# Optimization experiments

Hardware: AMD Instinct MI355X
Metric: run time of the kernel (lower is better)

## Reference

```python
import jax, jax.numpy as jnp
import numpy as np

B, D_IN, LAT, C = 16384, 512, 64, 8
HID = [1024, 512, 256]

def _lin(k, fi, fo, scale=0.02):
    k1, k2 = jax.random.split(k)
    return jax.random.normal(k1, (fi, fo), jnp.float32) * scale, jax.random.normal(k2, (fo,), jnp.float32) * scale

def _lin_c(k, fi, fo, scale=0.02):
    k1, k2 = jax.random.split(k)
    return jax.random.normal(k1, (C, fi, fo), jnp.float32) * scale, jax.random.normal(k2, (C, fo), jnp.float32) * scale

def setup_inputs() -> dict:
    key = jax.random.key(0)
    ks = jax.random.split(key, 16)
    x = jax.random.normal(ks[0], (B, D_IN), jnp.float32)
    cluster_labels = jax.random.randint(ks[1], (B,), 0, C, jnp.int32)
    eps = jax.random.normal(ks[2], (B, LAT), jnp.float32)
    # encoder: shared(512->1024), unshared(1024->512), shared(512->256)
    enc_W0, enc_b0 = _lin(ks[3], D_IN, HID[0])
    enc_Wu, enc_bu = _lin_c(ks[4], HID[0], HID[1])
    enc_W2, enc_b2 = _lin(ks[5], HID[1], HID[2])
    # shared latent heads
    mu_W, mu_b = _lin(ks[6], HID[2], LAT)
    lv_W, lv_b = _lin(ks[7], HID[2], LAT)
    # decoder (hidden_dims reversed = [256,512,1024]): unshared(64->256), shared(256->512), unshared(512->1024)
    dec_Wu0, dec_bu0 = _lin_c(ks[8], LAT, HID[2])
    dec_W1, dec_b1 = _lin(ks[9], HID[2], HID[1])
    dec_Wu2, dec_bu2 = _lin_c(ks[10], HID[1], HID[0])
    # per-cluster final layer (1024 -> input_dim), no activation (all-continuous)
    fin_W, fin_b = _lin_c(ks[11], HID[0], D_IN)
    return dict(x=x, cluster_labels=cluster_labels, eps=eps,
                enc_W0=enc_W0, enc_b0=enc_b0, enc_Wu=enc_Wu, enc_bu=enc_bu,
                enc_W2=enc_W2, enc_b2=enc_b2, mu_W=mu_W, mu_b=mu_b,
                lv_W=lv_W, lv_b=lv_b, dec_Wu0=dec_Wu0, dec_bu0=dec_bu0,
                dec_W1=dec_W1, dec_b1=dec_b1, dec_Wu2=dec_Wu2, dec_bu2=dec_bu2,
                fin_W=fin_W, fin_b=fin_b)

def _unshared(h, W, b, labels):
    # per-cluster GEMM then row-wise combine (mask-based dispatch, no row reorder)
    y = jnp.einsum('bi,cio->bco', h, W) + b[None]  # [B, C, out]
    return jnp.take_along_axis(y, labels[:, None, None], axis=1)[:, 0, :]

def reference(x, cluster_labels, eps,
              enc_W0, enc_b0, enc_Wu, enc_bu, enc_W2, enc_b2,
              mu_W, mu_b, lv_W, lv_b,
              dec_Wu0, dec_bu0, dec_W1, dec_b1, dec_Wu2, dec_bu2,
              fin_W, fin_b):
    lbl = cluster_labels.astype(jnp.int32)
    # encoder
    h = jax.nn.relu(x @ enc_W0 + enc_b0)
    h = jax.nn.relu(_unshared(h, enc_Wu, enc_bu, lbl))
    h = jax.nn.relu(h @ enc_W2 + enc_b2)
    mu = h @ mu_W + mu_b
    logvar = h @ lv_W + lv_b
    # reparameterize
    z = mu + jnp.exp(0.5 * logvar) * eps
    # decoder
    h = jax.nn.relu(_unshared(z, dec_Wu0, dec_bu0, lbl))
    h = jax.nn.relu(h @ dec_W1 + dec_b1)
    h = jax.nn.relu(_unshared(h, dec_Wu2, dec_bu2, lbl))
    # per-cluster final output layer (identity activation: all-continuous)
    recon = _unshared(h, fin_W, fin_b, lbl)
    return recon
```

## Files before the change

kernel.cpp:

```cpp
#include <hip/hip_runtime.h>

typedef _Float16 f16;
typedef __attribute__((ext_vector_type(8))) _Float16 f16x8;
typedef __attribute__((ext_vector_type(4))) _Float16 f16x4;
typedef __attribute__((ext_vector_type(4))) float    f32x4;

#define B_ROWS 16384
#define MPAD   18432
#define MT256  72
#define MT128  144
#define NBLK   64

typedef __attribute__((address_space(1))) void as1_void;
typedef __attribute__((address_space(3))) void as3_void;

__device__ __forceinline__ void gl_lds16(const void* g, void* l) {
    __builtin_amdgcn_global_load_lds((const as1_void*)g, (as3_void*)l, 16, 0, 0);
}


__global__ __launch_bounds__(256) void k_prep(const int* __restrict__ lbl, int* __restrict__ blockhist,
                                              int* __restrict__ rowmap,
                                              const float* __restrict__ mb_, const float* __restrict__ lb_,
                                              float* __restrict__ bz, f16* __restrict__ zerob) {
    int b = blockIdx.x, t = threadIdx.x;
    int i = b * 256 + t;
    rowmap[i] = -1;
    if (b < NBLK) {
        __shared__ int h[8];
        if (t < 8) h[t] = 0;
        __syncthreads();
        atomicAdd(&h[lbl[i]], 1);
        __syncthreads();
        if (t < 8) blockhist[b * 8 + t] = h[t];
    } else if (b == NBLK) {
        if (t < 64) zerob[t] = (f16)0.f;
        if (t < 64) bz[t] = mb_[t];
        else if (t < 128) bz[t] = lb_[t - 64];
    }
}

__global__ void k_offsets(const int* __restrict__ blockhist, int* offs, int* tilec256, int* tilec128,
                          int* blockbase) {
    __shared__ int tot[8];
    __shared__ int so[9];
    int t = threadIdx.x;
    if (t < 8) {
        int s = 0;
        for (int b = 0; b < NBLK; ++b) s += blockhist[b * 8 + t];
        tot[t] = s;
    }
    __syncthreads();
    if (t == 0) {
        int o = 0;
        for (int c = 0; c < 8; ++c) { so[c] = o; o += (tot[c] + 255) & ~255; }
        so[8] = o;
        for (int c = 0; c < 9; ++c) offs[c] = so[c];
    }
    __syncthreads();
    if (t < 8) {
        int run = so[t];
        for (int b = 0; b < NBLK; ++b) {
            blockbase[b * 8 + t] = run;
            run += blockhist[b * 8 + t];
        }
    }
    if (t < MT256) {
        int row = t * 256, c = 7;
        for (int cc = 0; cc < 8; ++cc)
            if (row >= so[cc] && row < so[cc + 1]) c = cc;
        tilec256[t] = c;
    }
    if (t < MT128) {
        int row = t * 128, c = 7;
        for (int cc = 0; cc < 8; ++cc)
            if (row >= so[cc] && row < so[cc + 1]) c = cc;
        tilec128[t] = c;
    }
}

__global__ __launch_bounds__(256) void k_scatter(const int* __restrict__ lbl,
                                                 const int* __restrict__ blockbase,
                                                 int* __restrict__ rowmap) {
    __shared__ int cur[8];
    if (threadIdx.x < 8) cur[threadIdx.x] = blockbase[blockIdx.x * 8 + threadIdx.x];
    __syncthreads();
    int i = blockIdx.x * 256 + threadIdx.x;
    int c = lbl[i];
    int pos = atomicAdd(&cur[c], 1);
    rowmap[pos] = i;
}


struct Seg { const float* s; f16* d; int K, N, b0, nx, ny; long sCS, dCS; };
struct SegTab { Seg g[10]; };

__global__ __launch_bounds__(256) void k_trans(SegTab tab, const float* __restrict__ x, f16* __restrict__ xh) {
    int bid = blockIdx.x;
    int t = threadIdx.x;
    if (bid < tab.g[1].b0) {
        long i = (long)bid * 256 + t;
        const float4* xs = (const float4*)x;
        float4 v0 = xs[i * 2], v1 = xs[i * 2 + 1];
        f16x8 o = {(f16)v0.x, (f16)v0.y, (f16)v0.z, (f16)v0.w,
                   (f16)v1.x, (f16)v1.y, (f16)v1.z, (f16)v1.w};
        ((f16x8*)xh)[i] = o;
        return;
    }
    int s = 9;
    while (bid < tab.g[s].b0) --s;
    Seg sg = tab.g[s];
    int lb = bid - sg.b0;
    int nxy = sg.nx * sg.ny;
    int z = lb / nxy; int r = lb - z * nxy;
    int by = r / sg.nx; int bx = r - by * sg.nx;
    const float* src = sg.s + (size_t)z * sg.sCS;
    f16* dst = sg.d + (size_t)z * sg.dCS;
    int k0 = by * 64, n0 = bx * 64;

    __shared__ f16 tr[64][88];
    int a = t & 15, b = t >> 4;
    float4 v[4];
    #pragma unroll
    for (int i = 0; i < 4; ++i)
        v[i] = *(const float4*)&src[(size_t)(k0 + b * 4 + i) * sg.N + n0 + a * 4];
    #pragma unroll
    for (int j = 0; j < 4; ++j) {
        f16x4 w = {(f16)((const float*)&v[0])[j], (f16)((const float*)&v[1])[j],
                   (f16)((const float*)&v[2])[j], (f16)((const float*)&v[3])[j]};
        *(f16x4*)&tr[a * 4 + j][b * 4] = w;
    }
    __syncthreads();
    int n = t >> 2, s4 = t & 3;
    f16x8 o0 = *(const f16x8*)&tr[n][s4 * 16];
    f16x8 o1 = *(const f16x8*)&tr[n][s4 * 16 + 8];
    *(f16x8*)&dst[(size_t)(n0 + n) * sg.K + k0 + s4 * 16] = o0;
    *(f16x8*)&dst[(size_t)(n0 + n) * sg.K + k0 + s4 * 16 + 8] = o1;
}

__global__ __launch_bounds__(256) void k_reparam(const f16* __restrict__ muv, const float* __restrict__ eps,
                                                 const int* __restrict__ rowmap, f16* __restrict__ z) {
    int i = blockIdx.x * 256 + threadIdx.x;
    int p = i >> 6, j = i & 63;
    int g = rowmap[p];
    float e  = (g >= 0) ? eps[(size_t)g * 64 + j] : 0.f;
    float mu = (float)muv[(size_t)p * 128 + j];
    float lv = (float)muv[(size_t)p * 128 + 64 + j];
    z[i] = (f16)(mu + expf(0.5f * lv) * e);
}


template<int GATHER, int PERW, int RELU, int SCATTER>
__global__ __launch_bounds__(512, 2) void gemm2(
    const f16* __restrict__ A, const f16* __restrict__ Wt,
    const float* __restrict__ bias, f16* __restrict__ Out, float* __restrict__ OutF,
    const int* __restrict__ rowmap, const int* __restrict__ tilec,
    const f16* __restrict__ zerobuf, int K, int N)
{
    __shared__ __align__(16) f16 lA[2][256 * 32];
    __shared__ __align__(16) f16 lB[2][256 * 32];
    const int tid  = threadIdx.x;
    const int wave = tid >> 6;
    const int lane = tid & 63;

    const int id  = blockIdx.x;
    const int xcd = id & 7;
    const int jj  = id >> 3;
    const int tm  = (jj % 9) * 8 + xcd;
    const int tn  = jj / 9;
    const int r0 = tm * 256, n0 = tn * 256;

    const f16* wb = Wt;
    const float* bb = bias;
    if (PERW) {
        int c = tilec[tm];
        wb += (size_t)c * K * N;
        bb += (size_t)c * N;
    }

    const int srow = tid >> 2;
    const int sg   = tid & 3;
    const int xk16 = (sg ^ (srow & 3)) * 16;

    const char* pa[2]; size_t stepA[2];
    #pragma unroll
    for (int p = 0; p < 2; ++p) {
        int gr = r0 + p * 128 + srow;
        if (GATHER) {
            int g = rowmap[gr];
            if (g >= 0) { pa[p] = (const char*)(A + (size_t)g * K) + xk16; stepA[p] = 64; }
            else        { pa[p] = (const char*)zerobuf;                    stepA[p] = 0;  }
        } else {
            pa[p] = (const char*)(A + (size_t)gr * K) + xk16; stepA[p] = 64;
        }
    }
    const char* pb[2];
    #pragma unroll
    for (int p = 0; p < 2; ++p)
        pb[p] = (const char*)(wb + (size_t)(n0 + p * 128 + srow) * K) + xk16;

    const int wm = wave & 3, wn = wave >> 2;
    const int mb = wm * 64, nb = wn * 128;
    const int quad = lane >> 4;
    const int r16  = lane & 15;
    const int key  = r16 & 3;

    f32x4 acc[4][8];
    #pragma unroll
    for (int i = 0; i < 4; ++i)
        #pragma unroll
        for (int j = 0; j < 8; ++j)
            acc[i][j] = (f32x4){0.f, 0.f, 0.f, 0.f};

    const int nk = K >> 5;

    #pragma unroll
    for (int p = 0; p < 2; ++p) {
        gl_lds16(pa[p], (char*)lA[0] + p * 8192 + wave * 1024);
        gl_lds16(pb[p], (char*)lB[0] + p * 8192 + wave * 1024);
        pa[p] += stepA[p]; pb[p] += 64;
    }

    for (int kb = 0; kb < nk; ++kb) {
        const int cur = kb & 1, nxt = cur ^ 1;
        __syncthreads();
        if (kb + 1 < nk) {
            #pragma unroll
            for (int p = 0; p < 2; ++p) {
                gl_lds16(pa[p], (char*)lA[nxt] + p * 8192 + wave * 1024);
                gl_lds16(pb[p], (char*)lB[nxt] + p * 8192 + wave * 1024);
                pa[p] += stepA[p]; pb[p] += 64;
            }
        }
        f16x8 af[4], bf[8];
        #pragma unroll
        for (int i = 0; i < 4; ++i)
            af[i] = *(const f16x8*)((const char*)lA[cur] + (mb + i * 16 + r16) * 64 + ((quad ^ key) * 16));
        #pragma unroll
        for (int j = 0; j < 8; ++j)
            bf[j] = *(const f16x8*)((const char*)lB[cur] + (nb + j * 16 + r16) * 64 + ((quad ^ key) * 16));
        #pragma unroll
        for (int i = 0; i < 4; ++i)
            #pragma unroll
            for (int j = 0; j < 8; ++j)
                acc[i][j] = __builtin_amdgcn_mfma_f32_16x16x32_f16(af[i], bf[j], acc[i][j], 0, 0, 0);
    }

    float bv[8];
    #pragma unroll
    for (int j = 0; j < 8; ++j) bv[j] = bb[n0 + nb + j * 16 + r16];

    #pragma unroll
    for (int i = 0; i < 4; ++i) {
        #pragma unroll
        for (int r = 0; r < 4; ++r) {
            int orow = r0 + mb + i * 16 + quad * 4 + r;
            int g = 0;
            if (SCATTER) g = rowmap[orow];
            #pragma unroll
            for (int j = 0; j < 8; ++j) {
                int ocol = n0 + nb + j * 16 + r16;
                float v = acc[i][j][r] + bv[j];
                if (RELU) v = fmaxf(v, 0.f);
                if (SCATTER) {
                    if (g >= 0) OutF[(size_t)g * N + ocol] = v;
                } else {
                    Out[(size_t)orow * N + ocol] = (f16)v;
                }
            }
        }
    }
}


template<int GATHER, int PERW, int RELU, int SCATTER>
__global__ __launch_bounds__(256, 2) void gemm_k(
    const f16* __restrict__ A, const f16* __restrict__ Wt,
    const float* __restrict__ bias, f16* __restrict__ Out, float* __restrict__ OutF,
    const int* __restrict__ rowmap, const int* __restrict__ tilec,
    const f16* __restrict__ zerobuf, int K, int N)
{
    __shared__ __align__(16) f16 lA[2][128 * 64];
    __shared__ __align__(16) f16 lB[2][128 * 64];
    const int tid  = threadIdx.x;
    const int wave = tid >> 6;
    const int lane = tid & 63;

    const int id  = blockIdx.x;
    const int xcd = id & 7;
    const int jj  = id >> 3;
    const int tm  = (jj % 18) * 8 + xcd;
    const int tn  = jj / 18;
    const int r0 = tm * 128, n0 = tn * 128;

    const f16* wb = Wt;
    const float* bb = bias;
    if (PERW) {
        int c = tilec[tm];
        wb += (size_t)c * K * N;
        bb += (size_t)c * N;
    }

    const int srow = tid >> 3;
    const int sg   = tid & 7;
    const int xk16 = (sg ^ (srow & 7)) * 16;
    const size_t rowB = (size_t)K * 2;
    const size_t passB = 32 * rowB;

    const char* pa[4]; size_t stepA[4];
    #pragma unroll
    for (int p = 0; p < 4; ++p) {
        int gr = r0 + p * 32 + srow;
        if (GATHER) {
            int g = rowmap[gr];
            if (g >= 0) { pa[p] = (const char*)(A + (size_t)g * K) + xk16; stepA[p] = 128; }
            else        { pa[p] = (const char*)zerobuf;                    stepA[p] = 0;   }
        } else {
            pa[p] = (const char*)(A + (size_t)gr * K) + xk16; stepA[p] = 128;
        }
    }
    const char* pb = (const char*)(wb + (size_t)(n0 + srow) * K) + xk16;

    const int mb = (wave >> 1) * 64;
    const int nb = (wave & 1) * 64;
    const int quad = lane >> 4;
    const int r16  = lane & 15;
    const int key  = r16 & 7;

    f32x4 acc[4][4];
    #pragma unroll
    for (int i = 0; i < 4; ++i)
        #pragma unroll
        for (int j = 0; j < 4; ++j)
            acc[i][j] = (f32x4){0.f, 0.f, 0.f, 0.f};

    const int nk = K >> 6;

    #pragma unroll
    for (int p = 0; p < 4; ++p)
        gl_lds16(pa[p], (char*)lA[0] + p * 4096 + wave * 1024);
    #pragma unroll
    for (int p = 0; p < 4; ++p)
        gl_lds16(pb + p * passB, (char*)lB[0] + p * 4096 + wave * 1024);
    #pragma unroll
    for (int p = 0; p < 4; ++p) pa[p] += stepA[p];
    pb += 128;

    for (int kb = 0; kb < nk; ++kb) {
        const int cur = kb & 1, nxt = cur ^ 1;
        __syncthreads();
        if (kb + 1 < nk) {
            #pragma unroll
            for (int p = 0; p < 4; ++p)
                gl_lds16(pa[p], (char*)lA[nxt] + p * 4096 + wave * 1024);
            #pragma unroll
            for (int p = 0; p < 4; ++p)
                gl_lds16(pb + p * passB, (char*)lB[nxt] + p * 4096 + wave * 1024);
            #pragma unroll
            for (int p = 0; p < 4; ++p) pa[p] += stepA[p];
            pb += 128;
        }
        #pragma unroll
        for (int kk = 0; kk < 2; ++kk) {
            const int off = ((kk * 4 + quad) ^ key) * 16;
            f16x8 af[4], bf[4];
            #pragma unroll
            for (int i = 0; i < 4; ++i)
                af[i] = *(const f16x8*)((const char*)lA[cur] + (mb + i * 16 + r16) * 128 + off);
            #pragma unroll
            for (int j = 0; j < 4; ++j)
                bf[j] = *(const f16x8*)((const char*)lB[cur] + (nb + j * 16 + r16) * 128 + off);
            #pragma unroll
            for (int i = 0; i < 4; ++i)
                #pragma unroll
                for (int j = 0; j < 4; ++j)
                    acc[i][j] = __builtin_amdgcn_mfma_f32_16x16x32_f16(af[i], bf[j], acc[i][j], 0, 0, 0);
        }
    }

    float bv[4];
    #pragma unroll
    for (int j = 0; j < 4; ++j) bv[j] = bb[n0 + nb + j * 16 + r16];

    #pragma unroll
    for (int i = 0; i < 4; ++i) {
        #pragma unroll
        for (int r = 0; r < 4; ++r) {
            int orow = r0 + mb + i * 16 + quad * 4 + r;
            int g = 0;
            if (SCATTER) g = rowmap[orow];
            #pragma unroll
            for (int j = 0; j < 4; ++j) {
                int ocol = n0 + nb + j * 16 + r16;
                float v = acc[i][j][r] + bv[j];
                if (RELU) v = fmaxf(v, 0.f);
                if (SCATTER) {
                    if (g >= 0) OutF[(size_t)g * N + ocol] = v;
                } else {
                    Out[(size_t)orow * N + ocol] = (f16)v;
                }
            }
        }
    }
}


extern "C" void kernel_launch(void* const* d_in, const int* in_sizes, int n_in,
                              void* d_out, int out_size, void* d_ws, size_t ws_size,
                              hipStream_t stream) {
    const float* x      = (const float*)d_in[0];
    const int*   lbl    = (const int*)  d_in[1];
    const float* eps    = (const float*)d_in[2];
    const float* enc_W0 = (const float*)d_in[3];
    const float* enc_b0 = (const float*)d_in[4];
    const float* enc_Wu = (const float*)d_in[5];
    const float* enc_bu = (const float*)d_in[6];
    const float* enc_W2 = (const float*)d_in[7];
    const float* enc_b2 = (const float*)d_in[8];
    const float* mu_W   = (const float*)d_in[9];
    const float* mu_b   = (const float*)d_in[10];
    const float* lv_W   = (const float*)d_in[11];
    const float* lv_b   = (const float*)d_in[12];
    const float* dWu0   = (const float*)d_in[13];
    const float* dbu0   = (const float*)d_in[14];
    const float* dW1    = (const float*)d_in[15];
    const float* db1    = (const float*)d_in[16];
    const float* dWu2   = (const float*)d_in[17];
    const float* dbu2   = (const float*)d_in[18];
    const float* finW   = (const float*)d_in[19];
    const float* finb   = (const float*)d_in[20];
    float* out = (float*)d_out;
    (void)in_sizes; (void)n_in; (void)out_size; (void)ws_size;

    char* base = (char*)d_ws;
    size_t off = 0;
    auto alloc = [&](size_t bytes) { char* r = base + off; off = (off + bytes + 255) & ~(size_t)255; return r; };
    f16* xh     = (f16*)alloc((size_t)B_ROWS * 512 * 2);
    f16* buf1   = (f16*)alloc((size_t)MPAD * 1024 * 2);
    f16* buf2   = (f16*)alloc((size_t)MPAD * 512 * 2);
    f16* buf3   = (f16*)alloc((size_t)MPAD * 256 * 2);
    f16* muv    = (f16*)alloc((size_t)MPAD * 128 * 2);
    f16* zb     = (f16*)alloc((size_t)MPAD * 64 * 2);
    f16* w0t    = (f16*)alloc(1024ul * 512 * 2);
    f16* wut    = (f16*)alloc(8ul * 512 * 1024 * 2);
    f16* w2t    = (f16*)alloc(256ul * 512 * 2);
    f16* wzt    = (f16*)alloc(128ul * 256 * 2);
    f16* wd0t   = (f16*)alloc(8ul * 256 * 64 * 2);
    f16* wd1t   = (f16*)alloc(512ul * 256 * 2);
    f16* wd2t   = (f16*)alloc(8ul * 1024 * 512 * 2);
    f16* wft    = (f16*)alloc(8ul * 512 * 1024 * 2);
    float* bz   = (float*)alloc(128 * 4);
    int* rowmap = (int*)alloc(MPAD * 4);
    int* blockhist = (int*)alloc(NBLK * 8 * 4);
    int* blockbase = (int*)alloc(NBLK * 8 * 4);
    int* offs   = (int*)alloc(64);
    int* tilec256 = (int*)alloc(MT256 * 4);
    int* tilec128 = (int*)alloc(MT128 * 4);
    f16* zerob  = (f16*)alloc(256);

    k_prep<<<MPAD / 256, 256, 0, stream>>>(lbl, blockhist, rowmap, mu_b, lv_b, bz, zerob);
    k_offsets<<<1, 256, 0, stream>>>(blockhist, offs, tilec256, tilec128, blockbase);
    k_scatter<<<NBLK, 256, 0, stream>>>(lbl, blockbase, rowmap);

    SegTab tab;
    int b0 = B_ROWS * 512 / 8 / 256;
    auto seg = [&](int i, const float* s, f16* d, int K, int N, int nz, long sCS, long dCS) {
        int nx = N / 64, ny = K / 64;
        tab.g[i] = Seg{s, d, K, N, b0, nx, ny, sCS, dCS};
        b0 += nx * ny * nz;
    };
    tab.g[0] = Seg{nullptr, nullptr, 0, 0, 0, 0, 0, 0, 0};
    seg(1, enc_W0, w0t, 512, 1024, 1, 0, 0);
    seg(2, enc_Wu, wut, 1024, 512, 8, 1024l * 512, 512l * 1024);
    seg(3, enc_W2, w2t, 512, 256, 1, 0, 0);
    seg(4, mu_W, wzt, 256, 64, 1, 0, 0);
    seg(5, lv_W, wzt + 64 * 256, 256, 64, 1, 0, 0);
    seg(6, dWu0, wd0t, 64, 256, 8, 64l * 256, 256l * 64);
    seg(7, dW1, wd1t, 256, 512, 1, 0, 0);
    seg(8, dWu2, wd2t, 512, 1024, 8, 512l * 1024, 1024l * 512);
    seg(9, finW, wft, 1024, 512, 8, 1024l * 512, 512l * 1024);
    k_trans<<<b0, 256, 0, stream>>>(tab, x, xh);

    gemm2<1,0,1,0><<<MT256 * 4, 512, 0, stream>>>(xh,   w0t,  enc_b0, buf1, nullptr, rowmap, tilec256, zerob, 512, 1024);
    gemm2<0,1,1,0><<<MT256 * 2, 512, 0, stream>>>(buf1, wut,  enc_bu, buf2, nullptr, rowmap, tilec256, zerob, 1024, 512);
    gemm2<0,0,1,0><<<MT256 * 1, 512, 0, stream>>>(buf2, w2t,  enc_b2, buf3, nullptr, rowmap, tilec256, zerob, 512, 256);
    gemm_k<0,0,0,0><<<MT128 * 1, 256, 0, stream>>>(buf3, wzt,  bz,     muv,  nullptr, rowmap, tilec128, zerob, 256, 128);
    k_reparam<<<MPAD * 64 / 256, 256, 0, stream>>>(muv, eps, rowmap, zb);
    gemm_k<0,1,1,0><<<MT128 * 2, 256, 0, stream>>>(zb,   wd0t, dbu0,   buf3, nullptr, rowmap, tilec128, zerob, 64, 256);
    gemm2<0,0,1,0><<<MT256 * 2, 512, 0, stream>>>(buf3, wd1t, db1,    buf2, nullptr, rowmap, tilec256, zerob, 256, 512);
    gemm2<0,1,1,0><<<MT256 * 4, 512, 0, stream>>>(buf2, wd2t, dbu2,   buf1, nullptr, rowmap, tilec256, zerob, 512, 1024);
    gemm2<0,1,0,1><<<MT256 * 2, 512, 0, stream>>>(buf1, wft,  finb,   nullptr, out,  rowmap, tilec256, zerob, 1024, 512);
}
```

Baseline: 425.1 us.

## Shrink M tile to 128 rows and reduce per-cluster padding

The 256x256 GEMM with 512 threads becomes a 128x256 tile with 256 threads. Per-cluster row padding drops from 256 to 128, so the padded row count falls from 18432 to 17408 and fewer wasted rows are computed. Block-to-tile mapping now places N tiles on fixed XCDs, so those tiles share weight panels in L2. Each block keeps the same 4x8 MFMA register tile per wave. The smaller tile gives less reuse of weights per block, in exchange for less padding waste and smaller per-block LDS.

Measured after the change: 394.7 us. 7.2% less time.

```diff
diff --git a/kernel.cpp b/kernel.cpp
--- a/kernel.cpp
+++ b/kernel.cpp
@@ -6,9 +6,8 @@
 typedef __attribute__((ext_vector_type(4))) float    f32x4;
 
 #define B_ROWS 16384
-#define MPAD   18432
-#define MT256  72
-#define MT128  144
+#define MPAD   17408
+#define MT     136
 #define NBLK   64
 
 typedef __attribute__((address_space(1))) void as1_void;
@@ -40,8 +39,7 @@
     }
 }
 
-__global__ void k_offsets(const int* __restrict__ blockhist, int* offs, int* tilec256, int* tilec128,
-                          int* blockbase) {
+__global__ void k_offsets(const int* __restrict__ blockhist, int* offs, int* tilec, int* blockbase) {
     __shared__ int tot[8];
     __shared__ int so[9];
     int t = threadIdx.x;
@@ -53,7 +51,7 @@
     __syncthreads();
     if (t == 0) {
         int o = 0;
-        for (int c = 0; c < 8; ++c) { so[c] = o; o += (tot[c] + 255) & ~255; }
+        for (int c = 0; c < 8; ++c) { so[c] = o; o += (tot[c] + 127) & ~127; }
         so[8] = o;
         for (int c = 0; c < 9; ++c) offs[c] = so[c];
     }
@@ -65,17 +63,11 @@
             run += blockhist[b * 8 + t];
         }
     }
-    if (t < MT256) {
-        int row = t * 256, c = 7;
-        for (int cc = 0; cc < 8; ++cc)
-            if (row >= so[cc] && row < so[cc + 1]) c = cc;
-        tilec256[t] = c;
-    }
-    if (t < MT128) {
+    if (t < MT) {
         int row = t * 128, c = 7;
         for (int cc = 0; cc < 8; ++cc)
             if (row >= so[cc] && row < so[cc + 1]) c = cc;
-        tilec128[t] = c;
+        tilec[t] = c;
     }
 }
 
@@ -150,14 +142,14 @@
 }
 
 
-template<int GATHER, int PERW, int RELU, int SCATTER>
-__global__ __launch_bounds__(512, 2) void gemm2(
+template<int GATHER, int PERW, int RELU, int SCATTER, int NTN>
+__global__ __launch_bounds__(256, 2) void gemm3(
     const f16* __restrict__ A, const f16* __restrict__ Wt,
     const float* __restrict__ bias, f16* __restrict__ Out, float* __restrict__ OutF,
     const int* __restrict__ rowmap, const int* __restrict__ tilec,
     const f16* __restrict__ zerobuf, int K, int N)
 {
-    __shared__ __align__(16) f16 lA[2][256 * 32];
+    __shared__ __align__(16) f16 lA[2][128 * 32];
     __shared__ __align__(16) f16 lB[2][256 * 32];
     const int tid  = threadIdx.x;
     const int wave = tid >> 6;
@@ -166,9 +158,10 @@
     const int id  = blockIdx.x;
     const int xcd = id & 7;
     const int jj  = id >> 3;
-    const int tm  = (jj % 9) * 8 + xcd;
-    const int tn  = jj / 9;
-    const int r0 = tm * 256, n0 = tn * 256;
+    const int XPT = 8 / NTN;
+    const int tn  = xcd / XPT;
+    const int tm  = jj * XPT + (xcd % XPT);
+    const int r0 = tm * 128, n0 = tn * 256;
 
     const f16* wb = Wt;
     const float* bb = bias;
@@ -185,7 +178,7 @@
     const char* pa[2]; size_t stepA[2];
     #pragma unroll
     for (int p = 0; p < 2; ++p) {
-        int gr = r0 + p * 128 + srow;
+        int gr = r0 + p * 64 + srow;
         if (GATHER) {
             int g = rowmap[gr];
             if (g >= 0) { pa[p] = (const char*)(A + (size_t)g * K) + xk16; stepA[p] = 64; }
@@ -194,16 +187,16 @@
             pa[p] = (const char*)(A + (size_t)gr * K) + xk16; stepA[p] = 64;
         }
     }
-    const char* pb[2];
-    #pragma unroll
-    for (int p = 0; p < 2; ++p)
-        pb[p] = (const char*)(wb + (size_t)(n0 + p * 128 + srow) * K) + xk16;
-
-    const int wm = wave & 3, wn = wave >> 2;
-    const int mb = wm * 64, nb = wn * 128;
+    const char* pb[4];
+    #pragma unroll
+    for (int p = 0; p < 4; ++p)
+        pb[p] = (const char*)(wb + (size_t)(n0 + p * 64 + srow) * K) + xk16;
+
+    const int mb = (wave & 1) * 64;
+    const int nb = (wave >> 1) * 128;
     const int quad = lane >> 4;
     const int r16  = lane & 15;
-    const int key  = r16 & 3;
+    const int off  = ((quad ^ (r16 & 3)) * 16);
 
     f32x4 acc[4][8];
     #pragma unroll
@@ -216,9 +209,13 @@
 
     #pragma unroll
     for (int p = 0; p < 2; ++p) {
-        gl_lds16(pa[p], (char*)lA[0] + p * 8192 + wave * 1024);
-        gl_lds16(pb[p], (char*)lB[0] + p * 8192 + wave * 1024);
-        pa[p] += stepA[p]; pb[p] += 64;
+        gl_lds16(pa[p], (char*)lA[0] + p * 4096 + wave * 1024);
+        pa[p] += stepA[p];
+    }
+    #pragma unroll
+    for (int p = 0; p < 4; ++p) {
+        gl_lds16(pb[p], (char*)lB[0] + p * 4096 + wave * 1024);
+        pb[p] += 64;
     }
 
     for (int kb = 0; kb < nk; ++kb) {
@@ -227,18 +224,22 @@
         if (kb + 1 < nk) {
             #pragma unroll
             for (int p = 0; p < 2; ++p) {
-                gl_lds16(pa[p], (char*)lA[nxt] + p * 8192 + wave * 1024);
-                gl_lds16(pb[p], (char*)lB[nxt] + p * 8192 + wave * 1024);
-                pa[p] += stepA[p]; pb[p] += 64;
+                gl_lds16(pa[p], (char*)lA[nxt] + p * 4096 + wave * 1024);
+                pa[p] += stepA[p];
             }
+            #pragma unroll
+            for (int p = 0; p < 4; ++p) {
+                gl_lds16(pb[p], (char*)lB[nxt] + p * 4096 + wave * 1024);
+                pb[p] += 64;
+            }
         }
         f16x8 af[4], bf[8];
         #pragma unroll
         for (int i = 0; i < 4; ++i)
-            af[i] = *(const f16x8*)((const char*)lA[cur] + (mb + i * 16 + r16) * 64 + ((quad ^ key) * 16));
+            af[i] = *(const f16x8*)((const char*)lA[cur] + (mb + i * 16 + r16) * 64 + off);
         #pragma unroll
         for (int j = 0; j < 8; ++j)
-            bf[j] = *(const f16x8*)((const char*)lB[cur] + (nb + j * 16 + r16) * 64 + ((quad ^ key) * 16));
+            bf[j] = *(const f16x8*)((const char*)lB[cur] + (nb + j * 16 + r16) * 64 + off);
         #pragma unroll
         for (int i = 0; i < 4; ++i)
             #pragma unroll
@@ -273,7 +274,7 @@
 }
 
 
-template<int GATHER, int PERW, int RELU, int SCATTER>
+template<int GATHER, int PERW, int RELU, int SCATTER, int NTN>
 __global__ __launch_bounds__(256, 2) void gemm_k(
     const f16* __restrict__ A, const f16* __restrict__ Wt,
     const float* __restrict__ bias, f16* __restrict__ Out, float* __restrict__ OutF,
@@ -289,8 +290,9 @@
     const int id  = blockIdx.x;
     const int xcd = id & 7;
     const int jj  = id >> 3;
-    const int tm  = (jj % 18) * 8 + xcd;
-    const int tn  = jj / 18;
+    const int XPT = 8 / NTN;
+    const int tn  = xcd / XPT;
+    const int tm  = jj * XPT + (xcd % XPT);
     const int r0 = tm * 128, n0 = tn * 128;
 
     const f16* wb = Wt;
@@ -454,12 +456,11 @@
     int* blockhist = (int*)alloc(NBLK * 8 * 4);
     int* blockbase = (int*)alloc(NBLK * 8 * 4);
     int* offs   = (int*)alloc(64);
-    int* tilec256 = (int*)alloc(MT256 * 4);
-    int* tilec128 = (int*)alloc(MT128 * 4);
+    int* tilec  = (int*)alloc(MT * 4);
     f16* zerob  = (f16*)alloc(256);
 
     k_prep<<<MPAD / 256, 256, 0, stream>>>(lbl, blockhist, rowmap, mu_b, lv_b, bz, zerob);
-    k_offsets<<<1, 256, 0, stream>>>(blockhist, offs, tilec256, tilec128, blockbase);
+    k_offsets<<<1, 256, 0, stream>>>(blockhist, offs, tilec, blockbase);
     k_scatter<<<NBLK, 256, 0, stream>>>(lbl, blockbase, rowmap);
 
     SegTab tab;
@@ -481,13 +482,13 @@
     seg(9, finW, wft, 1024, 512, 8, 1024l * 512, 512l * 1024);
     k_trans<<<b0, 256, 0, stream>>>(tab, x, xh);
 
-    gemm2<1,0,1,0><<<MT256 * 4, 512, 0, stream>>>(xh,   w0t,  enc_b0, buf1, nullptr, rowmap, tilec256, zerob, 512, 1024);
-    gemm2<0,1,1,0><<<MT256 * 2, 512, 0, stream>>>(buf1, wut,  enc_bu, buf2, nullptr, rowmap, tilec256, zerob, 1024, 512);
-    gemm2<0,0,1,0><<<MT256 * 1, 512, 0, stream>>>(buf2, w2t,  enc_b2, buf3, nullptr, rowmap, tilec256, zerob, 512, 256);
-    gemm_k<0,0,0,0><<<MT128 * 1, 256, 0, stream>>>(buf3, wzt,  bz,     muv,  nullptr, rowmap, tilec128, zerob, 256, 128);
+    gemm3<1,0,1,0,4><<<MT * 4, 256, 0, stream>>>(xh,   w0t,  enc_b0, buf1, nullptr, rowmap, tilec, zerob, 512, 1024);
+    gemm3<0,1,1,0,2><<<MT * 2, 256, 0, stream>>>(buf1, wut,  enc_bu, buf2, nullptr, rowmap, tilec, zerob, 1024, 512);
+    gemm3<0,0,1,0,1><<<MT * 1, 256, 0, stream>>>(buf2, w2t,  enc_b2, buf3, nullptr, rowmap, tilec, zerob, 512, 256);
+    gemm_k<0,0,0,0,1><<<MT * 1, 256, 0, stream>>>(buf3, wzt,  bz,    muv,  nullptr, rowmap, tilec, zerob, 256, 128);
     k_reparam<<<MPAD * 64 / 256, 256, 0, stream>>>(muv, eps, rowmap, zb);
-    gemm_k<0,1,1,0><<<MT128 * 2, 256, 0, stream>>>(zb,   wd0t, dbu0,   buf3, nullptr, rowmap, tilec128, zerob, 64, 256);
-    gemm2<0,0,1,0><<<MT256 * 2, 512, 0, stream>>>(buf3, wd1t, db1,    buf2, nullptr, rowmap, tilec256, zerob, 256, 512);
-    gemm2<0,1,1,0><<<MT256 * 4, 512, 0, stream>>>(buf2, wd2t, dbu2,   buf1, nullptr, rowmap, tilec256, zerob, 512, 1024);
-    gemm2<0,1,0,1><<<MT256 * 2, 512, 0, stream>>>(buf1, wft,  finb,   nullptr, out,  rowmap, tilec256, zerob, 1024, 512);
-}
+    gemm_k<0,1,1,0,2><<<MT * 2, 256, 0, stream>>>(zb,   wd0t, dbu0,  buf3, nullptr, rowmap, tilec, zerob, 64, 256);
+    gemm3<0,0,1,0,2><<<MT * 2, 256, 0, stream>>>(buf3, wd1t, db1,    buf2, nullptr, rowmap, tilec, zerob, 256, 512);
+    gemm3<0,1,1,0,4><<<MT * 4, 256, 0, stream>>>(buf2, wd2t, dbu2,   buf1, nullptr, rowmap, tilec, zerob, 512, 1024);
+    gemm3<0,1,0,1,2><<<MT * 2, 256, 0, stream>>>(buf1, wft,  finb,   nullptr, out,  rowmap, tilec, zerob, 1024, 512);
+}
```
